# Kernel tuning notes

Measured on AMD Instinct MI355X. Metric: run time of the kernel, lower is better.

## Reference

```python
import jax, jax.numpy as jnp
import numpy as np

N_NODES = 20000
N_EDGES = 640000
MUL = 32      # multiplicity of the 0e and 1o node-feature irreps
ATTR = 8      # node attr scalars (0e)
RBASIS = 16   # radial edge embedding size (0e)
FC_HID = 64   # radial MLP hidden size
AVG_NEIGH = 32.0
LOG2 = 0.6931471805599453


def _ssp(x):
    # ShiftedSoftPlus: softplus(x) - log(2)
    return jax.nn.softplus(x) - LOG2


def setup_inputs() -> dict:
    key = jax.random.key(0)
    ks = jax.random.split(key, 16)
    return {
        "node_s": jax.random.normal(ks[0], (N_NODES, MUL), jnp.float32),
        "node_v": jax.random.normal(ks[1], (N_NODES, MUL, 3), jnp.float32),
        "node_attrs": jax.random.uniform(ks[2], (N_NODES, ATTR), dtype=jnp.float32),
        "edge_emb": jax.random.normal(ks[3], (N_EDGES, RBASIS), jnp.float32),
        "edge_y0": jnp.ones((N_EDGES, 1), jnp.float32),  # Y_0 spherical harmonic is constant
        "edge_y1": jax.random.normal(ks[4], (N_EDGES, 3), jnp.float32),
        "edge_index": jax.random.randint(ks[5], (2, N_EDGES), 0, N_NODES, jnp.int32),
        "W1s": jax.random.normal(ks[6], (MUL, MUL), jnp.float32),
        "W1v": jax.random.normal(ks[7], (MUL, MUL), jnp.float32),
        "Wr1": jax.random.normal(ks[8], (RBASIS, FC_HID), jnp.float32),
        "Wr2": jax.random.normal(ks[9], (FC_HID, 4 * MUL), jnp.float32),
        "W2s": jax.random.normal(ks[10], (2 * MUL, MUL), jnp.float32),
        "W2v": jax.random.normal(ks[11], (2 * MUL, MUL), jnp.float32),
        "Wscs": jax.random.normal(ks[12], (MUL, ATTR, MUL), jnp.float32),
        "Wscv": jax.random.normal(ks[13], (MUL, ATTR, MUL), jnp.float32),
    }


def reference(node_s, node_v, node_attrs, edge_emb, edge_y0, edge_y1, edge_index,
              W1s, W1v, Wr1, Wr2, W2s, W2v, Wscs, Wscv):
    n = node_s.shape[0]
    src, dst = edge_index[0], edge_index[1]

    # linear_1 (e3nn Linear: per-irrep channel mixing, / sqrt(fan_in))
    inv_m = 1.0 / jnp.sqrt(jnp.float32(MUL))
    s = (node_s @ W1s) * inv_m                              # [N, MUL] 0e
    v = jnp.einsum('nui,uw->nwi', node_v, W1v) * inv_m      # [N, MUL, 3] 1o

    # radial MLP -> per-edge tensor-product weights (4 paths x MUL)
    h = _ssp((edge_emb @ Wr1) / jnp.sqrt(jnp.float32(RBASIS)))
    w = (h @ Wr2) / jnp.sqrt(jnp.float32(FC_HID))           # [E, 4*MUL]
    w1, w2, w3, w4 = jnp.split(w, 4, axis=1)

    # gather source node features
    se = s[src]                                             # [E, MUL]
    ve = v[src]                                             # [E, MUL, 3]

    # CG 'uvu' tensor product (sorted mid irreps: 0e(0ex0e), 0e(1ox1o), 1o(0ex1o), 1o(1ox0e))
    inv_sqrt3 = 1.0 / jnp.sqrt(3.0)
    mid_s = jnp.concatenate([
        w1 * se * edge_y0,                                          # 0e x 0e -> 0e
        w4 * jnp.einsum('eui,ei->eu', ve, edge_y1) * inv_sqrt3,     # 1o x 1o -> 0e
    ], axis=1)                                              # [E, 2*MUL]
    mid_v = jnp.concatenate([
        (w2 * se)[:, :, None] * edge_y1[:, None, :],                # 0e x 1o -> 1o
        w3[:, :, None] * ve * edge_y0[:, :, None],                  # 1o x 0e -> 1o
    ], axis=1)                                              # [E, 2*MUL, 3]

    # scatter-sum to destination nodes, / sqrt(avg_num_neighbors)
    inv_deg = 1.0 / jnp.sqrt(jnp.float32(AVG_NEIGH))
    agg_s = jax.ops.segment_sum(mid_s, dst, num_segments=n) * inv_deg
    agg_v = jax.ops.segment_sum(mid_v, dst, num_segments=n) * inv_deg

    # linear_2
    inv_2m = 1.0 / jnp.sqrt(jnp.float32(2 * MUL))
    ns = (agg_s @ W2s) * inv_2m
    nv = jnp.einsum('nui,uw->nwi', agg_v, W2v) * inv_2m

    # self connection: FullyConnectedTensorProduct(node_feats_in, node_attrs)
    inv_fan = 1.0 / jnp.sqrt(jnp.float32(MUL * ATTR))
    sc_s = jnp.einsum('nu,nv,uvw->nw', node_s, node_attrs, Wscs) * inv_fan
    sc_v = jnp.einsum('nui,nv,uvw->nwi', node_v, node_attrs, Wscv) * inv_fan

    out_s = ns + sc_s                                       # [N, MUL]
    out_v = (nv + sc_v).reshape(n, 3 * MUL)                 # [N, 3*MUL]
    return jnp.concatenate([out_s, out_v], axis=1)          # [N, 4*MUL] flat irreps layout
```

## Files before the change

kernel.cpp:

```cpp
#include <hip/hip_runtime.h>
#include <math.h>

typedef short bf16x8 __attribute__((ext_vector_type(8)));
typedef short short2v __attribute__((ext_vector_type(2)));
typedef short short4v __attribute__((ext_vector_type(4)));
typedef float f32x4 __attribute__((ext_vector_type(4)));

__device__ __forceinline__ float sspf(float x) {
    return __logf(1.0f + __expf(x)) - 0.6931471805599453f;
}
__device__ __forceinline__ short f2b(float f) {
    union { float f; unsigned u; } c; c.f = f;
    unsigned r = c.u + 0x7fff + ((c.u >> 16) & 1);
    return (short)(r >> 16);
}
__device__ __forceinline__ float b2f(short s) {
    union { unsigned u; float f; } c; c.u = ((unsigned)(unsigned short)s) << 16;
    return c.f;
}
__device__ __forceinline__ int rlanei(int v, int l) {
    return __builtin_amdgcn_readlane(v, l);
}
__device__ __forceinline__ float rlanef(float v, int l) {
    return __uint_as_float(__builtin_amdgcn_readlane(__float_as_uint(v), l));
}
__device__ __forceinline__ bf16x8 pack8(float4 a, float4 b) {
    bf16x8 o;
    o[0] = f2b(a.x); o[1] = f2b(a.y); o[2] = f2b(a.z); o[3] = f2b(a.w);
    o[4] = f2b(b.x); o[5] = f2b(b.y); o[6] = f2b(b.z); o[7] = f2b(b.w);
    return o;
}

constexpr float INV_M      = 0.17677669529663687f;
constexpr float INV_R      = 0.25f;
constexpr float INV_H      = 0.125f;
constexpr float INV_2M_DEG = 0.125f * 0.17677669529663687f;
constexpr float INV_FAN    = 0.0625f;
constexpr float INV_SQRT3  = 0.5773502691896258f;

__global__ __launch_bounds__(256) void k_lin1h(
    const float* __restrict__ node_s, const float* __restrict__ node_v,
    const float* __restrict__ W1s, const float* __restrict__ W1v,
    short* __restrict__ feat, int N,
    const int* __restrict__ eidx, int* __restrict__ count, int E,
    float4* __restrict__ aggz, int nagg4, int nblin, int nbhist, int nbz,
    const float* __restrict__ W2s, const float* __restrict__ W2v,
    const float* __restrict__ Wscs, const float* __restrict__ Wscv,
    short* __restrict__ wsB)
{
    int b = blockIdx.x;
    int tid = threadIdx.x;
    if (b >= nblin + nbhist + nbz) {
        int i0 = (b - nblin - nbhist - nbz) * 1024 + tid;
        #pragma unroll
        for (int r = 0; r < 4; ++r) {
            int idx = i0 + r * 256;
            if (idx < 20480) {
                int f = idx >> 9, rem = idx & 511;
                int ln = rem >> 3, j = rem & 7;
                int qq = ln >> 4, lmm = ln & 15;
                const float* Wp; int nt, t; float sc;
                if (f < 4)       { Wp = W2s;  nt = f >> 1;              t = f & 1; sc = INV_2M_DEG; }
                else if (f < 8)  { int g = f - 4;  Wp = W2v;  nt = g >> 1; t = g & 1; sc = INV_2M_DEG; }
                else if (f < 24) { int g = f - 8;  Wp = Wscs; nt = g >> 3; t = g & 7; sc = INV_FAN; }
                else             { int g = f - 24; Wp = Wscv; nt = g >> 3; t = g & 7; sc = INV_FAN; }
                wsB[idx] = f2b(Wp[(t * 32 + qq * 8 + j) * 32 + nt * 16 + lmm] * sc);
            }
        }
        return;
    }
    if (b >= nblin + nbhist) {
        int i0 = (b - nblin - nbhist) * 1024 + tid;
        #pragma unroll
        for (int r = 0; r < 4; ++r) {
            int idx = i0 + r * 256;
            if (idx < nagg4) aggz[idx] = make_float4(0.f, 0.f, 0.f, 0.f);
        }
        return;
    }
    if (b >= nblin) {
        int e = (b - nblin) * 256 + tid;
        if (e < E) atomicAdd(&count[(eidx[E + e] << 2) | (e & 3)], 1);
        return;
    }
    __shared__ short sF[4 * 512];
    {
        int f = tid >> 6, ln = tid & 63;
        int q = ln >> 4, lm = ln & 15;
        int nt = f & 1;
        const float* Wp = (f < 2) ? W1s : W1v;
        short* d8 = &sF[tid * 8];
        #pragma unroll
        for (int j = 0; j < 8; ++j) {
            int k = q * 8 + j;
            d8[j] = f2b(Wp[k * 32 + nt * 16 + lm] * INV_M);
        }
    }
    __syncthreads();
    int lane = tid & 63, wv = tid >> 6;
    int q = lane >> 4, lm = lane & 15;
    int n0 = (b * 4 + wv) * 16;
    if (n0 >= N) return;
    int nr = n0 + lm;

    const float* nsp = node_s + (size_t)nr * 32;
    bf16x8 as8 = pack8(*(const float4*)(nsp + q * 8), *(const float4*)(nsp + q * 8 + 4));
    const float* nvp = node_v + (size_t)nr * 96;
    bf16x8 av8[3];
    #pragma unroll
    for (int i = 0; i < 3; ++i)
        #pragma unroll
        for (int j = 0; j < 8; ++j) av8[i][j] = f2b(nvp[(q * 8 + j) * 3 + i]);

    #pragma unroll
    for (int nt = 0; nt < 2; ++nt) {
        bf16x8 bs = *(const bf16x8*)&sF[(nt * 64 + lane) * 8];
        bf16x8 bv = *(const bf16x8*)&sF[((2 + nt) * 64 + lane) * 8];
        f32x4 sa = __builtin_amdgcn_mfma_f32_16x16x32_bf16(
            as8, bs, (f32x4){0.f, 0.f, 0.f, 0.f}, 0, 0, 0);
        f32x4 v0 = __builtin_amdgcn_mfma_f32_16x16x32_bf16(
            av8[0], bv, (f32x4){0.f, 0.f, 0.f, 0.f}, 0, 0, 0);
        f32x4 v1 = __builtin_amdgcn_mfma_f32_16x16x32_bf16(
            av8[1], bv, (f32x4){0.f, 0.f, 0.f, 0.f}, 0, 0, 0);
        f32x4 v2 = __builtin_amdgcn_mfma_f32_16x16x32_bf16(
            av8[2], bv, (f32x4){0.f, 0.f, 0.f, 0.f}, 0, 0, 0);
        #pragma unroll
        for (int r = 0; r < 4; ++r) {
            short4v o = {f2b(sa[r]), f2b(v0[r]), f2b(v1[r]), f2b(v2[r])};
            *(short4v*)&feat[(size_t)(n0 + q * 4 + r) * 128 + (nt * 16 + lm) * 4] = o;
        }
    }
}

__global__ __launch_bounds__(256) void k_scanA(
    const int* __restrict__ count, int* __restrict__ bsum, int M)
{
    int tid = threadIdx.x;
    int i = blockIdx.x * 256 + tid;
    int v = (i < M) ? count[i] : 0;
    int x = v;
    #pragma unroll
    for (int off = 1; off < 64; off <<= 1) x += __shfl_xor(x, off, 64);
    __shared__ int ws[4];
    int lane = tid & 63, wv = tid >> 6;
    if (lane == 0) ws[wv] = x;
    __syncthreads();
    if (tid == 0) bsum[blockIdx.x] = ws[0] + ws[1] + ws[2] + ws[3];
}

__global__ __launch_bounds__(256) void k_scanC(
    const int* __restrict__ count, const int* __restrict__ bsum,
    int* __restrict__ cursor, int M)
{
    int tid = threadIdx.x, bid = blockIdx.x;
    int lane = tid & 63, wv = tid >> 6;
    int p = 0;
    if (tid < bid) p = bsum[tid];
    if (tid + 256 < bid) p += bsum[tid + 256];
    #pragma unroll
    for (int off = 1; off < 64; off <<= 1) p += __shfl_xor(p, off, 64);
    __shared__ int rs[4];
    if (lane == 0) rs[wv] = p;
    __syncthreads();
    int boffv = rs[0] + rs[1] + rs[2] + rs[3];

    int i = bid * 256 + tid;
    int v = (i < M) ? count[i] : 0;
    int x = v;
    #pragma unroll
    for (int off = 1; off < 64; off <<= 1) {
        int y = __shfl_up(x, off, 64);
        if (lane >= off) x += y;
    }
    __shared__ int wsum[4];
    if (lane == 63) wsum[wv] = x;
    __syncthreads();
    int add = 0;
    #pragma unroll
    for (int w = 0; w < 3; ++w) if (w < wv) add += wsum[w];
    if (i < M) cursor[i] = x - v + add + boffv;
}

__global__ __launch_bounds__(256) void k_fill(
    const int* __restrict__ eidx, int* __restrict__ cursor,
    int2* __restrict__ epair, int E)
{
    int e = blockIdx.x * 256 + threadIdx.x;
    if (e < E) {
        int d = eidx[E + e];
        int s = eidx[e];
        int slot = atomicAdd(&cursor[(d << 2) | (e & 3)], 1);
        epair[slot] = make_int2(e, d | (s << 16));
    }
}

__global__ __launch_bounds__(256) void k_fused(
    const float* __restrict__ emb, const int2* __restrict__ epair,
    const float* __restrict__ y1,
    const float* __restrict__ Wr1, const float* __restrict__ Wr2,
    const short* __restrict__ feat,
    float* __restrict__ agg_s, float* __restrict__ agg_v, int E)
{
    __shared__ short sW1[4 * 512];
    __shared__ short hbuf[4][16 * 72];
    __shared__ int   wtl[4][64 * 17];

    int tid = threadIdx.x;
    {
        int f = tid >> 6, ln = tid & 63;
        int qq = ln >> 4, lmm = ln & 15;
        short* d8 = &sW1[(f * 64 + ln) * 8];
        #pragma unroll
        for (int j = 0; j < 8; ++j) {
            int k = qq * 8 + j;
            d8[j] = (k < 16) ? f2b(Wr1[k * 64 + f * 16 + lmm] * INV_R) : (short)0;
        }
    }
    __syncthreads();

    int lane = tid & 63, wv = tid >> 6;
    int q = lane >> 4, lm = lane & 15;
    int u = lane & 31;
    bool low = (lane < 32);

    bf16x8 wr2f[16];
    #pragma unroll
    for (int nt = 0; nt < 8; ++nt) {
        float sc = INV_H * ((nt >= 6) ? INV_SQRT3 : 1.0f);
        #pragma unroll
        for (int kc = 0; kc < 2; ++kc) {
            #pragma unroll
            for (int j = 0; j < 8; ++j) {
                int k = kc * 32 + q * 8 + j;
                wr2f[nt * 2 + kc][j] = f2b(Wr2[k * 128 + nt * 16 + lm] * sc);
            }
        }
    }

    short* hl = hbuf[wv];
    int* wli = wtl[wv];

    int base = blockIdx.x * 256 + wv * 64;
    if (base >= E) return;

    int2 nep = epair[base + lm];
    float4 pa = make_float4(0.f, 0.f, 0.f, 0.f);
    float4 pb = make_float4(0.f, 0.f, 0.f, 0.f);
    if (q < 2) {
        const float* ep = emb + (size_t)nep.x * 16 + q * 8;
        pa = *(const float4*)ep;
        pb = *(const float4*)(ep + 4);
    }
    float npk = (q < 3) ? y1[(size_t)nep.x * 3 + q] : 0.f;

    float accs = 0.f, acc0 = 0.f, acc1 = 0.f, acc2 = 0.f;
    int cur = -1;

    for (int ch = 0; ch < 4; ++ch) {
        int2 myep = nep;
        int meta = (lane < 16) ? (myep.y & 0xffff) : (int)(((unsigned)myep.y) >> 16);
        float pkm = npk;

        bf16x8 af = (bf16x8){0, 0, 0, 0, 0, 0, 0, 0};
        if (q < 2) af = pack8(pa, pb);

        short4v pg[16];
        #pragma unroll
        for (int k = 0; k < 16; ++k) {
            int sr = rlanei(meta, 16 + k);
            pg[k] = *(const short4v*)&feat[(size_t)sr * 128 + u * 4];
        }

        if (ch < 3) {
            nep = epair[base + ch * 16 + 16 + lm];
            if (q < 2) {
                const float* ep = emb + (size_t)nep.x * 16 + q * 8;
                pa = *(const float4*)ep;
                pb = *(const float4*)(ep + 4);
            }
            npk = (q < 3) ? y1[(size_t)nep.x * 3 + q] : 0.f;
        }

        #pragma unroll
        for (int nt = 0; nt < 4; ++nt) {
            bf16x8 bfr = *(const bf16x8*)&sW1[(nt * 64 + lane) * 8];
            f32x4 x = __builtin_amdgcn_mfma_f32_16x16x32_bf16(
                af, bfr, (f32x4){0.f, 0.f, 0.f, 0.f}, 0, 0, 0);
            #pragma unroll
            for (int r = 0; r < 4; ++r)
                hl[(q * 4 + r) * 72 + nt * 16 + lm] = f2b(sspf(x[r]));
        }

        bf16x8 ha = *(const bf16x8*)&hl[lm * 72 + q * 8];
        bf16x8 hb = *(const bf16x8*)&hl[lm * 72 + 32 + q * 8];
        #pragma unroll
        for (int pr = 0; pr < 4; ++pr) {
            int ntA = (pr & 1) | ((pr >> 1) << 2);
            int ntB = ntA + 2;
            f32x4 aA = __builtin_amdgcn_mfma_f32_16x16x32_bf16(
                ha, wr2f[ntA * 2], (f32x4){0.f, 0.f, 0.f, 0.f}, 0, 0, 0);
            aA = __builtin_amdgcn_mfma_f32_16x16x32_bf16(hb, wr2f[ntA * 2 + 1], aA, 0, 0, 0);
            f32x4 aB = __builtin_amdgcn_mfma_f32_16x16x32_bf16(
                ha, wr2f[ntB * 2], (f32x4){0.f, 0.f, 0.f, 0.f}, 0, 0, 0);
            aB = __builtin_amdgcn_mfma_f32_16x16x32_bf16(hb, wr2f[ntB * 2 + 1], aB, 0, 0, 0);
            int cp = (pr & 1) * 16 + lm + (pr >> 1) * 32;
            int* wp = &wli[cp * 17 + q * 4];
            #pragma unroll
            for (int r = 0; r < 4; ++r)
                wp[r] = (int)(((unsigned)(unsigned short)f2b(aA[r])) |
                              (((unsigned)(unsigned short)f2b(aB[r])) << 16));
        }

        #pragma unroll
        for (int i = 0; i < 16; ++i) {
            short4v g = pg[i];
            float se = b2f(g[0]), vx = b2f(g[1]), vy = b2f(g[2]), vz = b2f(g[3]);
            int d = rlanei(meta, i);
            if (d != cur) {
                if (cur >= 0) {
                    atomicAdd(&agg_s[(size_t)cur * 64 + lane], accs);
                    float* av = &agg_v[(size_t)cur * 192 + lane];
                    atomicAdd(av, acc0); atomicAdd(av + 64, acc1); atomicAdd(av + 128, acc2);
                }
                accs = acc0 = acc1 = acc2 = 0.f;
                cur = d;
            }
            unsigned wword = (unsigned)wli[lane * 17 + i];
            float la = __uint_as_float(wword << 16);
            float lb = __uint_as_float(wword & 0xffff0000u);
            float y1x = rlanef(pkm, i);
            float y1y = rlanef(pkm, 16 + i);
            float y1z = rlanef(pkm, 32 + i);
            float dot = vx * y1x + vy * y1y + vz * y1z;
            accs = fmaf(low ? la : lb, low ? se : dot, accs);
            float t = low ? lb * se : la;
            acc0 = fmaf(t, low ? y1x : vx, acc0);
            acc1 = fmaf(t, low ? y1y : vy, acc1);
            acc2 = fmaf(t, low ? y1z : vz, acc2);
        }
    }
    if (cur >= 0) {
        atomicAdd(&agg_s[(size_t)cur * 64 + lane], accs);
        float* av = &agg_v[(size_t)cur * 192 + lane];
        atomicAdd(av, acc0); atomicAdd(av + 64, acc1); atomicAdd(av + 128, acc2);
    }
}

__global__ __launch_bounds__(256) void k_out(
    const float* __restrict__ node_s, const float* __restrict__ node_v,
    const float* __restrict__ attrs,
    const float* __restrict__ agg_s, const float* __restrict__ agg_v,
    const short* __restrict__ wsB,
    float* __restrict__ out, int N)
{
    __shared__ int4 sB4[2560];
    int tid = threadIdx.x;
    {
        const int4* gw = (const int4*)wsB;
        for (int i = tid; i < 2560; i += 256) sB4[i] = gw[i];
    }
    __syncthreads();
    const short* sB = (const short*)sB4;

    int lane = tid & 63, wv = tid >> 6;
    int q = lane >> 4, lm = lane & 15;
    int n0 = (blockIdx.x * 4 + wv) * 16;
    if (n0 >= N) return;
    int nr = n0 + lm;

    float4 at0 = *(const float4*)(attrs + (size_t)nr * 8);
    float4 at1 = *(const float4*)(attrs + (size_t)nr * 8 + 4);
    float at[8] = {at0.x, at0.y, at0.z, at0.w, at1.x, at1.y, at1.z, at1.w};

    const float* asp = agg_s + (size_t)nr * 64;
    bf16x8 aS[2];
    #pragma unroll
    for (int kc = 0; kc < 2; ++kc)
        aS[kc] = pack8(*(const float4*)(asp + kc * 32 + q * 8),
                       *(const float4*)(asp + kc * 32 + q * 8 + 4));

    const float* nsp = node_s + (size_t)nr * 32;
    bf16x8 scs[8];
    #pragma unroll
    for (int t = 0; t < 8; ++t) {
        float nv_ = nsp[t * 4 + q];
        #pragma unroll
        for (int j = 0; j < 8; ++j) scs[t][j] = f2b(nv_ * at[j]);
    }

    #pragma unroll
    for (int nt = 0; nt < 2; ++nt) {
        f32x4 acc = (f32x4){0.f, 0.f, 0.f, 0.f};
        acc = __builtin_amdgcn_mfma_f32_16x16x32_bf16(
            aS[0], *(const bf16x8*)&sB[(nt * 2 + 0) * 512 + lane * 8], acc, 0, 0, 0);
        acc = __builtin_amdgcn_mfma_f32_16x16x32_bf16(
            aS[1], *(const bf16x8*)&sB[(nt * 2 + 1) * 512 + lane * 8], acc, 0, 0, 0);
        #pragma unroll
        for (int t = 0; t < 8; ++t)
            acc = __builtin_amdgcn_mfma_f32_16x16x32_bf16(
                scs[t], *(const bf16x8*)&sB[(8 + nt * 8 + t) * 512 + lane * 8], acc, 0, 0, 0);
        #pragma unroll
        for (int r = 0; r < 4; ++r)
            out[(size_t)(n0 + q * 4 + r) * 128 + nt * 16 + lm] = acc[r];
    }

    const float* nvp = node_v + (size_t)nr * 96;
    const float* avp = agg_v + (size_t)nr * 192;
    #pragma unroll
    for (int i = 0; i < 3; ++i) {
        bf16x8 aV[2];
        #pragma unroll
        for (int kc = 0; kc < 2; ++kc)
            aV[kc] = pack8(*(const float4*)(avp + i * 64 + kc * 32 + q * 8),
                           *(const float4*)(avp + i * 64 + kc * 32 + q * 8 + 4));
        bf16x8 scv[8];
        #pragma unroll
        for (int t = 0; t < 8; ++t) {
            float nv_ = nvp[(t * 4 + q) * 3 + i];
            #pragma unroll
            for (int j = 0; j < 8; ++j) scv[t][j] = f2b(nv_ * at[j]);
        }
        #pragma unroll
        for (int nt = 0; nt < 2; ++nt) {
            f32x4 acc = (f32x4){0.f, 0.f, 0.f, 0.f};
            acc = __builtin_amdgcn_mfma_f32_16x16x32_bf16(
                aV[0], *(const bf16x8*)&sB[(4 + nt * 2 + 0) * 512 + lane * 8], acc, 0, 0, 0);
            acc = __builtin_amdgcn_mfma_f32_16x16x32_bf16(
                aV[1], *(const bf16x8*)&sB[(4 + nt * 2 + 1) * 512 + lane * 8], acc, 0, 0, 0);
            #pragma unroll
            for (int t = 0; t < 8; ++t)
                acc = __builtin_amdgcn_mfma_f32_16x16x32_bf16(
                    scv[t], *(const bf16x8*)&sB[(24 + nt * 8 + t) * 512 + lane * 8], acc, 0, 0, 0);
            #pragma unroll
            for (int r = 0; r < 4; ++r)
                out[(size_t)(n0 + q * 4 + r) * 128 + 32 + (nt * 16 + lm) * 3 + i] = acc[r];
        }
    }
}

extern "C" void kernel_launch(void* const* d_in, const int* in_sizes, int n_in,
                              void* d_out, int out_size, void* d_ws, size_t ws_size,
                              hipStream_t stream)
{
    const float* node_s = (const float*)d_in[0];
    const float* node_v = (const float*)d_in[1];
    const float* attrs  = (const float*)d_in[2];
    const float* emb    = (const float*)d_in[3];
    const float* y1     = (const float*)d_in[5];
    const int*   eidx   = (const int*)d_in[6];
    const float* W1s  = (const float*)d_in[7];
    const float* W1v  = (const float*)d_in[8];
    const float* Wr1  = (const float*)d_in[9];
    const float* Wr2  = (const float*)d_in[10];
    const float* W2s  = (const float*)d_in[11];
    const float* W2v  = (const float*)d_in[12];
    const float* Wscs = (const float*)d_in[13];
    const float* Wscv = (const float*)d_in[14];

    int N = in_sizes[0] / 32;
    int E = in_sizes[3] / 16;

    float* agg_s = (float*)d_ws;
    float* agg_v = agg_s + (size_t)N * 64;
    short* feat  = (short*)(agg_v + (size_t)N * 192);
    int* count   = (int*)(feat + (size_t)N * 128);
    int* cursor  = count + (size_t)4 * N;
    int2* epair  = (int2*)(cursor + (size_t)4 * N);
    int* bsum    = (int*)(epair + E);
    short* wsB   = (short*)(bsum + 1024);

    hipMemsetAsync(count, 0, (size_t)4 * N * sizeof(int), stream);

    int M  = 4 * N;
    int NB = (M + 255) / 256;
    int nblin  = (N + 63) / 64;
    int nbhist = (E + 255) / 256;
    int nagg4  = N * 64;
    int nbz    = (nagg4 + 1023) / 1024;
    int nbw    = (20480 + 1023) / 1024;
    k_lin1h<<<dim3(nblin + nbhist + nbz + nbw), dim3(256), 0, stream>>>(
        node_s, node_v, W1s, W1v, feat, N,
        eidx, count, E, (float4*)agg_s, nagg4, nblin, nbhist, nbz,
        W2s, W2v, Wscs, Wscv, wsB);
    k_scanA<<<dim3(NB), dim3(256), 0, stream>>>(count, bsum, M);
    k_scanC<<<dim3(NB), dim3(256), 0, stream>>>(count, bsum, cursor, M);
    k_fill<<<dim3((E + 255) / 256), dim3(256), 0, stream>>>(eidx, cursor, epair, E);
    k_fused<<<dim3((E + 255) / 256), dim3(256), 0, stream>>>(emb, epair, y1,
                                                             Wr1, Wr2, feat,
                                                             agg_s, agg_v, E);
    k_out<<<dim3((N + 63) / 64), dim3(256), 0, stream>>>(node_s, node_v, attrs, agg_s, agg_v,
                                                         wsB, (float*)d_out, N);
}
```

Measured before the change: 323.9 us.

## Prepack Wr2 fragments in bf16 and stream them per chunk to cut registers

The bf16 conversion of the Wr2 MFMA fragments moves into the preprocessing kernel, which writes them to workspace. k_fused now reloads these fragments from global memory through volatile loads inside each chunk instead of keeping 16 bf16x8 fragments resident in registers. The feature gather prefetch is also shrunk from 16 to 8 entries in a rolling buffer that refills inside the accumulate loop. Together these lower register pressure to raise occupancy, at the cost of extra L1/L2 weight loads on every chunk.

```diff
diff --git a/kernel.cpp b/kernel.cpp
--- a/kernel.cpp
+++ b/kernel.cpp
@@ -5,6 +5,7 @@
 typedef short short2v __attribute__((ext_vector_type(2)));
 typedef short short4v __attribute__((ext_vector_type(4)));
 typedef float f32x4 __attribute__((ext_vector_type(4)));
+typedef int int4x __attribute__((ext_vector_type(4)));
 
 __device__ __forceinline__ float sspf(float x) {
     return __logf(1.0f + __expf(x)) - 0.6931471805599453f;
@@ -46,7 +47,7 @@
     float4* __restrict__ aggz, int nagg4, int nblin, int nbhist, int nbz,
     const float* __restrict__ W2s, const float* __restrict__ W2v,
     const float* __restrict__ Wscs, const float* __restrict__ Wscv,
-    short* __restrict__ wsB)
+    const float* __restrict__ Wr2, short* __restrict__ wsB)
 {
     int b = blockIdx.x;
     int tid = threadIdx.x;
@@ -65,6 +66,15 @@
                 else if (f < 24) { int g = f - 8;  Wp = Wscs; nt = g >> 3; t = g & 7; sc = INV_FAN; }
                 else             { int g = f - 24; Wp = Wscv; nt = g >> 3; t = g & 7; sc = INV_FAN; }
                 wsB[idx] = f2b(Wp[(t * 32 + qq * 8 + j) * 32 + nt * 16 + lmm] * sc);
+            } else if (idx < 36864) {
+                int i2 = idx - 20480;
+                int fr = i2 >> 9, rem = i2 & 511;
+                int ln = rem >> 3, j = rem & 7;
+                int qq = ln >> 4, lmm = ln & 15;
+                int kc = fr & 1, nt = fr >> 1;
+                int k = kc * 32 + qq * 8 + j;
+                float sc = INV_H * ((nt >= 6) ? INV_SQRT3 : 1.0f);
+                wsB[idx] = f2b(Wr2[k * 128 + nt * 16 + lmm] * sc);
             }
         }
         return;
@@ -197,7 +207,7 @@
 __global__ __launch_bounds__(256) void k_fused(
     const float* __restrict__ emb, const int2* __restrict__ epair,
     const float* __restrict__ y1,
-    const float* __restrict__ Wr1, const float* __restrict__ Wr2,
+    const float* __restrict__ Wr1, const short* __restrict__ wsW2,
     const short* __restrict__ feat,
     float* __restrict__ agg_s, float* __restrict__ agg_v, int E)
 {
@@ -223,25 +233,15 @@
     int u = lane & 31;
     bool low = (lane < 32);
 
-    bf16x8 wr2f[16];
-    #pragma unroll
-    for (int nt = 0; nt < 8; ++nt) {
-        float sc = INV_H * ((nt >= 6) ? INV_SQRT3 : 1.0f);
-        #pragma unroll
-        for (int kc = 0; kc < 2; ++kc) {
-            #pragma unroll
-            for (int j = 0; j < 8; ++j) {
-                int k = kc * 32 + q * 8 + j;
-                wr2f[nt * 2 + kc][j] = f2b(Wr2[k * 128 + nt * 16 + lm] * sc);
-            }
-        }
-    }
-
     short* hl = hbuf[wv];
     int* wli = wtl[wv];
 
     int base = blockIdx.x * 256 + wv * 64;
     if (base >= E) return;
+
+    const short* w2p = wsW2 + (size_t)lane * 8;
+#define LOADW(dst, fr) { int4x t_ = *(const volatile int4x*)&w2p[(fr) * 512]; \
+                         dst = *(bf16x8*)&t_; }
 
     int2 nep = epair[base + lm];
     float4 pa = make_float4(0.f, 0.f, 0.f, 0.f);
@@ -264,9 +264,9 @@
         bf16x8 af = (bf16x8){0, 0, 0, 0, 0, 0, 0, 0};
         if (q < 2) af = pack8(pa, pb);
 
-        short4v pg[16];
-        #pragma unroll
-        for (int k = 0; k < 16; ++k) {
+        short4v pg[8];
+        #pragma unroll
+        for (int k = 0; k < 8; ++k) {
             int sr = rlanei(meta, 16 + k);
             pg[k] = *(const short4v*)&feat[(size_t)sr * 128 + u * 4];
         }
@@ -293,27 +293,73 @@
 
         bf16x8 ha = *(const bf16x8*)&hl[lm * 72 + q * 8];
         bf16x8 hb = *(const bf16x8*)&hl[lm * 72 + 32 + q * 8];
-        #pragma unroll
-        for (int pr = 0; pr < 4; ++pr) {
-            int ntA = (pr & 1) | ((pr >> 1) << 2);
-            int ntB = ntA + 2;
-            f32x4 aA = __builtin_amdgcn_mfma_f32_16x16x32_bf16(
-                ha, wr2f[ntA * 2], (f32x4){0.f, 0.f, 0.f, 0.f}, 0, 0, 0);
-            aA = __builtin_amdgcn_mfma_f32_16x16x32_bf16(hb, wr2f[ntA * 2 + 1], aA, 0, 0, 0);
-            f32x4 aB = __builtin_amdgcn_mfma_f32_16x16x32_bf16(
-                ha, wr2f[ntB * 2], (f32x4){0.f, 0.f, 0.f, 0.f}, 0, 0, 0);
-            aB = __builtin_amdgcn_mfma_f32_16x16x32_bf16(hb, wr2f[ntB * 2 + 1], aB, 0, 0, 0);
-            int cp = (pr & 1) * 16 + lm + (pr >> 1) * 32;
-            int* wp = &wli[cp * 17 + q * 4];
-            #pragma unroll
-            for (int r = 0; r < 4; ++r)
-                wp[r] = (int)(((unsigned)(unsigned short)f2b(aA[r])) |
-                              (((unsigned)(unsigned short)f2b(aB[r])) << 16));
+        {
+            bf16x8 c0, c1, c2, c3, n0, n1, n2, n3;
+            LOADW(c0, 0)  LOADW(c1, 1)  LOADW(c2, 4)  LOADW(c3, 5)
+            LOADW(n0, 2)  LOADW(n1, 3)  LOADW(n2, 6)  LOADW(n3, 7)
+            {
+                f32x4 aA = __builtin_amdgcn_mfma_f32_16x16x32_bf16(
+                    ha, c0, (f32x4){0.f, 0.f, 0.f, 0.f}, 0, 0, 0);
+                aA = __builtin_amdgcn_mfma_f32_16x16x32_bf16(hb, c1, aA, 0, 0, 0);
+                f32x4 aB = __builtin_amdgcn_mfma_f32_16x16x32_bf16(
+                    ha, c2, (f32x4){0.f, 0.f, 0.f, 0.f}, 0, 0, 0);
+                aB = __builtin_amdgcn_mfma_f32_16x16x32_bf16(hb, c3, aB, 0, 0, 0);
+                int* wp = &wli[(0 * 16 + lm + 0 * 32) * 17 + q * 4];
+                #pragma unroll
+                for (int r = 0; r < 4; ++r)
+                    wp[r] = (int)(((unsigned)(unsigned short)f2b(aA[r])) |
+                                  (((unsigned)(unsigned short)f2b(aB[r])) << 16));
+            }
+            LOADW(c0, 8)  LOADW(c1, 9)  LOADW(c2, 12)  LOADW(c3, 13)
+            {
+                f32x4 aA = __builtin_amdgcn_mfma_f32_16x16x32_bf16(
+                    ha, n0, (f32x4){0.f, 0.f, 0.f, 0.f}, 0, 0, 0);
+                aA = __builtin_amdgcn_mfma_f32_16x16x32_bf16(hb, n1, aA, 0, 0, 0);
+                f32x4 aB = __builtin_amdgcn_mfma_f32_16x16x32_bf16(
+                    ha, n2, (f32x4){0.f, 0.f, 0.f, 0.f}, 0, 0, 0);
+                aB = __builtin_amdgcn_mfma_f32_16x16x32_bf16(hb, n3, aB, 0, 0, 0);
+                int* wp = &wli[(1 * 16 + lm + 0 * 32) * 17 + q * 4];
+                #pragma unroll
+                for (int r = 0; r < 4; ++r)
+                    wp[r] = (int)(((unsigned)(unsigned short)f2b(aA[r])) |
+                                  (((unsigned)(unsigned short)f2b(aB[r])) << 16));
+            }
+            LOADW(n0, 10)  LOADW(n1, 11)  LOADW(n2, 14)  LOADW(n3, 15)
+            {
+                f32x4 aA = __builtin_amdgcn_mfma_f32_16x16x32_bf16(
+                    ha, c0, (f32x4){0.f, 0.f, 0.f, 0.f}, 0, 0, 0);
+                aA = __builtin_amdgcn_mfma_f32_16x16x32_bf16(hb, c1, aA, 0, 0, 0);
+                f32x4 aB = __builtin_amdgcn_mfma_f32_16x16x32_bf16(
+                    ha, c2, (f32x4){0.f, 0.f, 0.f, 0.f}, 0, 0, 0);
+                aB = __builtin_amdgcn_mfma_f32_16x16x32_bf16(hb, c3, aB, 0, 0, 0);
+                int* wp = &wli[(0 * 16 + lm + 1 * 32) * 17 + q * 4];
+                #pragma unroll
+                for (int r = 0; r < 4; ++r)
+                    wp[r] = (int)(((unsigned)(unsigned short)f2b(aA[r])) |
+                                  (((unsigned)(unsigned short)f2b(aB[r])) << 16));
+            }
+            {
+                f32x4 aA = __builtin_amdgcn_mfma_f32_16x16x32_bf16(
+                    ha, n0, (f32x4){0.f, 0.f, 0.f, 0.f}, 0, 0, 0);
+                aA = __builtin_amdgcn_mfma_f32_16x16x32_bf16(hb, n1, aA, 0, 0, 0);
+                f32x4 aB = __builtin_amdgcn_mfma_f32_16x16x32_bf16(
+                    ha, n2, (f32x4){0.f, 0.f, 0.f, 0.f}, 0, 0, 0);
+                aB = __builtin_amdgcn_mfma_f32_16x16x32_bf16(hb, n3, aB, 0, 0, 0);
+                int* wp = &wli[(1 * 16 + lm + 1 * 32) * 17 + q * 4];
+                #pragma unroll
+                for (int r = 0; r < 4; ++r)
+                    wp[r] = (int)(((unsigned)(unsigned short)f2b(aA[r])) |
+                                  (((unsigned)(unsigned short)f2b(aB[r])) << 16));
+            }
         }
 
         #pragma unroll
         for (int i = 0; i < 16; ++i) {
-            short4v g = pg[i];
+            short4v g = pg[i & 7];
+            if (i + 8 < 16) {
+                int sr = rlanei(meta, 16 + i + 8);
+                pg[(i + 8) & 7] = *(const short4v*)&feat[(size_t)sr * 128 + u * 4];
+            }
             float se = b2f(g[0]), vx = b2f(g[1]), vy = b2f(g[2]), vz = b2f(g[3]);
             int d = rlanei(meta, i);
             if (d != cur) {
@@ -339,6 +385,7 @@
             acc2 = fmaf(t, low ? y1z : vz, acc2);
         }
     }
+#undef LOADW
     if (cur >= 0) {
         atomicAdd(&agg_s[(size_t)cur * 64 + lane], accs);
         float* av = &agg_v[(size_t)cur * 192 + lane];
@@ -468,8 +515,9 @@
     int2* epair  = (int2*)(cursor + (size_t)4 * N);
     int* bsum    = (int*)(epair + E);
     short* wsB   = (short*)(bsum + 1024);
-
-    hipMemsetAsync(count, 0, (size_t)4 * N * sizeof(int), stream);
+    short* wsW2  = wsB + 20480;
+
+    (void)hipMemsetAsync(count, 0, (size_t)4 * N * sizeof(int), stream);
 
     int M  = 4 * N;
     int NB = (M + 255) / 256;
@@ -477,16 +525,16 @@
     int nbhist = (E + 255) / 256;
     int nagg4  = N * 64;
     int nbz    = (nagg4 + 1023) / 1024;
-    int nbw    = (20480 + 1023) / 1024;
+    int nbw    = (36864 + 1023) / 1024;
     k_lin1h<<<dim3(nblin + nbhist + nbz + nbw), dim3(256), 0, stream>>>(
         node_s, node_v, W1s, W1v, feat, N,
         eidx, count, E, (float4*)agg_s, nagg4, nblin, nbhist, nbz,
-        W2s, W2v, Wscs, Wscv, wsB);
+        W2s, W2v, Wscs, Wscv, Wr2, wsB);
     k_scanA<<<dim3(NB), dim3(256), 0, stream>>>(count, bsum, M);
     k_scanC<<<dim3(NB), dim3(256), 0, stream>>>(count, bsum, cursor, M);
     k_fill<<<dim3((E + 255) / 256), dim3(256), 0, stream>>>(eidx, cursor, epair, E);
     k_fused<<<dim3((E + 255) / 256), dim3(256), 0, stream>>>(emb, epair, y1,
-                                                             Wr1, Wr2, feat,
+                                                             Wr1, wsW2, feat,
                                                              agg_s, agg_v, E);
     k_out<<<dim3((N + 63) / 64), dim3(256), 0, stream>>>(node_s, node_v, attrs, agg_s, agg_v,
                                                          wsB, (float*)d_out, N);
```

New measurement: 340.7 us. +5.2%, slower.

## Load source index in fused kernel, pipeline feature gathers, split weight tile

Applied to the files above, without the earlier changes.

k_fill now writes only the destination index into epair, and k_fused reads the source node from edge_index itself. This drops the 16-bit src/dst packing, which breaks once node ids reach 65536. The feature gather register array is cut from 16 to 8 entries and refilled inside the accumulation loop, which lowers register pressure and overlaps gathers with the FMA work. The per-edge weight tile in LDS becomes two separate bf16 short arrays written once per MFMA output, and the 1/sqrt3 scale moves from the Wr2 fragments to the MFMA outputs. In exchange it adds one extra scattered global load per edge, and the in-loop gathers may expose their latency.

```diff
diff --git a/kernel.cpp b/kernel.cpp
--- a/kernel.cpp
+++ b/kernel.cpp
@@ -188,14 +188,14 @@
     int e = blockIdx.x * 256 + threadIdx.x;
     if (e < E) {
         int d = eidx[E + e];
-        int s = eidx[e];
         int slot = atomicAdd(&cursor[(d << 2) | (e & 3)], 1);
-        epair[slot] = make_int2(e, d | (s << 16));
+        epair[slot] = make_int2(e, d);
     }
 }
 
 __global__ __launch_bounds__(256) void k_fused(
     const float* __restrict__ emb, const int2* __restrict__ epair,
+    const int* __restrict__ eidx,
     const float* __restrict__ y1,
     const float* __restrict__ Wr1, const float* __restrict__ Wr2,
     const short* __restrict__ feat,
@@ -203,7 +203,7 @@
 {
     __shared__ short sW1[4 * 512];
     __shared__ short hbuf[4][16 * 72];
-    __shared__ int   wtl[4][64 * 17];
+    __shared__ short wtl[4][2 * 64 * 18];
 
     int tid = threadIdx.x;
     {
@@ -226,19 +226,18 @@
     bf16x8 wr2f[16];
     #pragma unroll
     for (int nt = 0; nt < 8; ++nt) {
-        float sc = INV_H * ((nt >= 6) ? INV_SQRT3 : 1.0f);
         #pragma unroll
         for (int kc = 0; kc < 2; ++kc) {
             #pragma unroll
             for (int j = 0; j < 8; ++j) {
                 int k = kc * 32 + q * 8 + j;
-                wr2f[nt * 2 + kc][j] = f2b(Wr2[k * 128 + nt * 16 + lm] * sc);
+                wr2f[nt * 2 + kc][j] = f2b(Wr2[k * 128 + nt * 16 + lm] * INV_H);
             }
         }
     }
 
     short* hl = hbuf[wv];
-    int* wli = wtl[wv];
+    short* wl = wtl[wv];
 
     int base = blockIdx.x * 256 + wv * 64;
     if (base >= E) return;
@@ -251,6 +250,8 @@
         pa = *(const float4*)ep;
         pb = *(const float4*)(ep + 4);
     }
+    int nsrc = 0;
+    if (lane >= 16 && lane < 32) nsrc = eidx[nep.x];
     float npk = (q < 3) ? y1[(size_t)nep.x * 3 + q] : 0.f;
 
     float accs = 0.f, acc0 = 0.f, acc1 = 0.f, acc2 = 0.f;
@@ -258,15 +259,15 @@
 
     for (int ch = 0; ch < 4; ++ch) {
         int2 myep = nep;
-        int meta = (lane < 16) ? (myep.y & 0xffff) : (int)(((unsigned)myep.y) >> 16);
+        int meta = (lane < 16) ? myep.y : nsrc;
         float pkm = npk;
 
         bf16x8 af = (bf16x8){0, 0, 0, 0, 0, 0, 0, 0};
         if (q < 2) af = pack8(pa, pb);
 
-        short4v pg[16];
-        #pragma unroll
-        for (int k = 0; k < 16; ++k) {
+        short4v pg[8];
+        #pragma unroll
+        for (int k = 0; k < 8; ++k) {
             int sr = rlanei(meta, 16 + k);
             pg[k] = *(const short4v*)&feat[(size_t)sr * 128 + u * 4];
         }
@@ -278,6 +279,7 @@
                 pa = *(const float4*)ep;
                 pb = *(const float4*)(ep + 4);
             }
+            if (lane >= 16 && lane < 32) nsrc = eidx[nep.x];
             npk = (q < 3) ? y1[(size_t)nep.x * 3 + q] : 0.f;
         }
 
@@ -294,26 +296,27 @@
         bf16x8 ha = *(const bf16x8*)&hl[lm * 72 + q * 8];
         bf16x8 hb = *(const bf16x8*)&hl[lm * 72 + 32 + q * 8];
         #pragma unroll
-        for (int pr = 0; pr < 4; ++pr) {
-            int ntA = (pr & 1) | ((pr >> 1) << 2);
-            int ntB = ntA + 2;
-            f32x4 aA = __builtin_amdgcn_mfma_f32_16x16x32_bf16(
-                ha, wr2f[ntA * 2], (f32x4){0.f, 0.f, 0.f, 0.f}, 0, 0, 0);
-            aA = __builtin_amdgcn_mfma_f32_16x16x32_bf16(hb, wr2f[ntA * 2 + 1], aA, 0, 0, 0);
-            f32x4 aB = __builtin_amdgcn_mfma_f32_16x16x32_bf16(
-                ha, wr2f[ntB * 2], (f32x4){0.f, 0.f, 0.f, 0.f}, 0, 0, 0);
-            aB = __builtin_amdgcn_mfma_f32_16x16x32_bf16(hb, wr2f[ntB * 2 + 1], aB, 0, 0, 0);
-            int cp = (pr & 1) * 16 + lm + (pr >> 1) * 32;
-            int* wp = &wli[cp * 17 + q * 4];
-            #pragma unroll
-            for (int r = 0; r < 4; ++r)
-                wp[r] = (int)(((unsigned)(unsigned short)f2b(aA[r])) |
-                              (((unsigned)(unsigned short)f2b(aB[r])) << 16));
+        for (int nt = 0; nt < 8; ++nt) {
+            f32x4 acc = __builtin_amdgcn_mfma_f32_16x16x32_bf16(
+                ha, wr2f[nt * 2], (f32x4){0.f, 0.f, 0.f, 0.f}, 0, 0, 0);
+            acc = __builtin_amdgcn_mfma_f32_16x16x32_bf16(hb, wr2f[nt * 2 + 1], acc, 0, 0, 0);
+            float scl = (nt >= 6) ? INV_SQRT3 : 1.0f;
+            int cp = (nt & 1) * 16 + lm + ((nt >> 2) & 1) * 32;
+            int half = (nt >> 1) & 1;
+            short* wp = &wl[half * 1152 + cp * 18 + q * 4];
+            short2v p01 = {f2b(acc[0] * scl), f2b(acc[1] * scl)};
+            short2v p23 = {f2b(acc[2] * scl), f2b(acc[3] * scl)};
+            *(short2v*)&wp[0] = p01;
+            *(short2v*)&wp[2] = p23;
         }
 
         #pragma unroll
         for (int i = 0; i < 16; ++i) {
-            short4v g = pg[i];
+            short4v g = pg[i & 7];
+            if (i + 8 < 16) {
+                int sr = rlanei(meta, 16 + i + 8);
+                pg[(i + 8) & 7] = *(const short4v*)&feat[(size_t)sr * 128 + u * 4];
+            }
             float se = b2f(g[0]), vx = b2f(g[1]), vy = b2f(g[2]), vz = b2f(g[3]);
             int d = rlanei(meta, i);
             if (d != cur) {
@@ -325,9 +328,8 @@
                 accs = acc0 = acc1 = acc2 = 0.f;
                 cur = d;
             }
-            unsigned wword = (unsigned)wli[lane * 17 + i];
-            float la = __uint_as_float(wword << 16);
-            float lb = __uint_as_float(wword & 0xffff0000u);
+            float la = b2f(wl[lane * 18 + i]);
+            float lb = b2f(wl[1152 + lane * 18 + i]);
             float y1x = rlanef(pkm, i);
             float y1y = rlanef(pkm, 16 + i);
             float y1z = rlanef(pkm, 32 + i);
@@ -469,7 +471,7 @@
     int* bsum    = (int*)(epair + E);
     short* wsB   = (short*)(bsum + 1024);
 
-    hipMemsetAsync(count, 0, (size_t)4 * N * sizeof(int), stream);
+    (void)hipMemsetAsync(count, 0, (size_t)4 * N * sizeof(int), stream);
 
     int M  = 4 * N;
     int NB = (M + 255) / 256;
@@ -485,7 +487,7 @@
     k_scanA<<<dim3(NB), dim3(256), 0, stream>>>(count, bsum, M);
     k_scanC<<<dim3(NB), dim3(256), 0, stream>>>(count, bsum, cursor, M);
     k_fill<<<dim3((E + 255) / 256), dim3(256), 0, stream>>>(eidx, cursor, epair, E);
-    k_fused<<<dim3((E + 255) / 256), dim3(256), 0, stream>>>(emb, epair, y1,
+    k_fused<<<dim3((E + 255) / 256), dim3(256), 0, stream>>>(emb, epair, eidx, y1,
                                                              Wr1, Wr2, feat,
                                                              agg_s, agg_v, E);
     k_out<<<dim3((N + 63) / 64), dim3(256), 0, stream>>>(node_s, node_v, attrs, agg_s, agg_v,
```

Result: faster. 310.5 us (-4.1%).
